# Performance work log

Measured on AMD Instinct MI355X. Metric: run time of the kernel, lower is better.

Reference implementation:

```python
import jax, jax.numpy as jnp
import numpy as np

# Tap offsets (dy, dx) within the 3x3 footprint for each kernel_type.
# kernel_type 0 -> 5-tap skeleton (center + 4-neighbors), 1 -> full 3x3, else -> 3-tap row.
TAPS = {
    0: [(1, 1), (0, 1), (1, 0), (1, 2), (2, 1)],
    1: [(i, j) for i in range(3) for j in range(3)],
    2: [(1, 0), (1, 1), (1, 2)],
}

KERNEL_TYPE = 0
STRIDE = 1
PAD = 1
DIL = 1
SPATIAL = False


def setup_inputs() -> dict:
    key = jax.random.key(0)
    k1, k2 = jax.random.split(key)
    N, Ci, H, W = 16, 256, 64, 64
    Co, K = 256, len(TAPS[KERNEL_TYPE])
    x = jax.random.normal(k1, (N, Ci, H, W), dtype=jnp.float32)
    # kaiming-uniform-ish scale
    bound = np.sqrt(6.0 / (Ci * K))
    weight = jax.random.uniform(k2, (Co, Ci, K), dtype=jnp.float32, minval=-bound, maxval=bound)
    return {"x": x, "weight": weight, "step": 0}


def _spatial_conv(x, weight):
    # x: [N, Ci, H, W], weight: [Co, Ci, K]
    taps = TAPS[KERNEL_TYPE]
    N, Ci, H, W = x.shape
    Hout = (H + 2 * PAD - (DIL * 2 + 1)) // STRIDE + 1
    Wout = (W + 2 * PAD - (DIL * 2 + 1)) // STRIDE + 1
    xp = jnp.pad(x, ((0, 0), (0, 0), (PAD, PAD), (PAD, PAD)))
    outs = []
    for k, (dy, dx) in enumerate(taps):
        y0, x0 = dy * DIL, dx * DIL
        xs = xp[:, :, y0:y0 + (Hout - 1) * STRIDE + 1:STRIDE,
                      x0:x0 + (Wout - 1) * STRIDE + 1:STRIDE]  # [N, Ci, Hout, Wout]
        outs.append(jnp.einsum('nchw,oc->nohw', xs, weight[:, :, k]))
    return jnp.stack(outs, axis=0)  # [K, N, Co, Hout, Wout]


def reference(x, weight, step):
    out = _spatial_conv(x, weight)  # [K, N, Co, H, W]
    if SPATIAL:
        K, N, Co, Ho, Wo = out.shape
        out = jnp.transpose(out, (1, 0, 2, 3, 4)).reshape(N, K * Co, Ho, Wo)
    else:
        out = out.sum(axis=0)  # sum over taps -> [N, Co, H, W]
    return out
```

## Files before the change

kernel.cpp:

```cpp
#include <hip/hip_runtime.h>
#include <hip/hip_bf16.h>
#include <cstddef>

#define N_  16
#define CI  256
#define CO  256
#define KT  5

#define XBUF_B   16896
#define WOFF     33792
#define WBUF_B   40960
#define SMEM_B   115712

typedef __attribute__((ext_vector_type(8)))  short  short8;
typedef __attribute__((ext_vector_type(8)))  unsigned short ushort8;
typedef __attribute__((ext_vector_type(4)))  unsigned int uint4v;
typedef __attribute__((ext_vector_type(16))) float  floatx16;

static __device__ __forceinline__ unsigned short f2bf(float f) {
    union { float f; unsigned u; } v; v.f = f;
    unsigned r = v.u + 0x7fff + ((v.u >> 16) & 1);
    return (unsigned short)(r >> 16);
}

typedef const __attribute__((address_space(1))) unsigned int g_u32;
typedef __attribute__((address_space(3))) unsigned int l_u32;
static __device__ __forceinline__ void gload_lds16(const void* g, void* l) {
    __builtin_amdgcn_global_load_lds((g_u32*)g, (l_u32*)l, 16, 0, 0);
}

__global__ void wtrans_kernel(const float* __restrict__ w, unsigned short* __restrict__ wb) {
    int idx = blockIdx.x * 256 + threadIdx.x;
    if (idx >= KT * CO * CI) return;
    int e  = idx & 7;
    int o  = (idx >> 3) & 255;
    int lh = (idx >> 11) & 1;
    int ks = (idx >> 12) & 1;
    int c  = (idx >> 13) & 7;
    int k  = idx >> 16;
    int ci = c * 32 + ks * 16 + lh * 8 + e;
    wb[idx] = f2bf(w[(size_t)o * (CI * KT) + ci * KT + k]);
}

template<int KS>
static __device__ __forceinline__ void compute_half(const char* wB, const char* xB,
                                                    floatx16 (&acc)[2][2]) {
    #pragma unroll
    for (int k = 0; k < KT; ++k) {
        const int dy = (k == 1) ? 0 : (k == 4) ? 2 : 1;
        const int dx = (k == 2) ? 0 : (k == 3) ? 2 : 1;
        const short8 a0 = *(const short8*)(wB + k * 8192);
        const short8 a1 = *(const short8*)(wB + k * 8192 + 512);
        const short8 b0 = *(const short8*)(xB + (dy * 264 + KS * 132 + dx) * 16);
        const short8 b1 = *(const short8*)(xB + (dy * 264 + KS * 132 + 32 + dx) * 16);
        acc[0][0] = __builtin_amdgcn_mfma_f32_32x32x16_bf16(a0, b0, acc[0][0], 0, 0, 0);
        acc[1][0] = __builtin_amdgcn_mfma_f32_32x32x16_bf16(a1, b0, acc[1][0], 0, 0, 0);
        acc[0][1] = __builtin_amdgcn_mfma_f32_32x32x16_bf16(a0, b1, acc[0][1], 0, 0, 0);
        acc[1][1] = __builtin_amdgcn_mfma_f32_32x32x16_bf16(a1, b1, acc[1][1], 0, 0, 0);
    }
}

__global__ __launch_bounds__(512, 2) void conv_mfma(const float* __restrict__ x,
                                                    const unsigned short* __restrict__ wb,
                                                    float* __restrict__ out) {
    extern __shared__ char smem[];

    const int tid = threadIdx.x;
    const int bx0 = blockIdx.x;
    const int bx  = (bx0 & 7) * 64 + (bx0 >> 3);
    const int g   = bx & 31;
    const int n   = bx >> 5;
    const int h0  = g * 2;

    const int lane  = tid & 63;
    const int wv    = tid >> 6;
    const int l31   = lane & 31;
    const int lh    = lane >> 5;
    const int owave = (wv & 3) * 64;
    const int hrow  = wv >> 2;

    const int sw  = tid & 63;
    const int scg = (tid >> 6) & 3;
    const int sr2 = tid >> 8;

    if (tid < 64) {
        int buf = tid & 1;
        int wp  = ((tid >> 1) & 1) * 65;
        int cg  = (tid >> 2) & 3;
        int r   = (tid >> 4) & 3;
        ((ushort8*)smem)[buf * 1056 + r * 264 + cg * 66 + wp] = (ushort8)0;
    }

    const float* xn = x + (size_t)n * CI * 4096;

    float zm[2];
    int   hcl[2];
    #pragma unroll
    for (int ii = 0; ii < 2; ++ii) {
        int hh = h0 - 1 + sr2 * 2 + ii;
        zm[ii]  = ((unsigned)hh < 64u) ? 1.f : 0.f;
        hcl[ii] = hh < 0 ? 0 : (hh > 63 ? 63 : hh);
    }

    float xr[2][8];
    auto load_chunk = [&](int c) {
        #pragma unroll
        for (int ii = 0; ii < 2; ++ii) {
            const float* p = xn + (c * 32 + scg * 8) * 4096 + hcl[ii] * 64 + sw;
            #pragma unroll
            for (int e = 0; e < 8; ++e) xr[ii][e] = p[e * 4096];
        }
    };
    auto write_chunk = [&](int b) {
        #pragma unroll
        for (int ii = 0; ii < 2; ++ii) {
            const int i = sr2 * 2 + ii;
            uint4v v;
            #pragma unroll
            for (int e = 0; e < 4; ++e) {
                __hip_bfloat162 pk = __float22bfloat162_rn(
                    make_float2(zm[ii] * xr[ii][2 * e], zm[ii] * xr[ii][2 * e + 1]));
                union { __hip_bfloat162 h; unsigned u; } cv; cv.h = pk;
                v[e] = cv.u;
            }
            *(uint4v*)&((ushort8*)smem)[b * 1056 + i * 264 + scg * 66 + (sw + 1)] = v;
        }
    };
    auto stage_w = [&](int c, int ks, int buf) {
        const char* src = (const char*)wb + c * 16384 + ks * 8192 + wv * 1024 + lane * 16;
        char* dst = smem + WOFF + buf * WBUF_B + wv * 1024;
        #pragma unroll
        for (int i = 0; i < 5; ++i)
            gload_lds16(src + (size_t)i * 131072, dst + i * 8192);
    };

    floatx16 acc[2][2];
    #pragma unroll
    for (int ot = 0; ot < 2; ++ot)
        #pragma unroll
        for (int t = 0; t < 2; ++t)
            #pragma unroll
            for (int e = 0; e < 16; ++e) acc[ot][t][e] = 0.f;

    const char* xbase = smem + hrow * 4224 + lh * 1056 + l31 * 16;
    const char* wbase = smem + WOFF + lh * 4096 + (owave + l31) * 16;

    stage_w(0, 0, 0);
    load_chunk(0);
    write_chunk(0);
    __builtin_amdgcn_sched_barrier(0);
    asm volatile("s_waitcnt vmcnt(0) lgkmcnt(0)" ::: "memory");
    __builtin_amdgcn_s_barrier();
    __builtin_amdgcn_sched_barrier(0);

    for (int c = 0; c < 8; ++c) {
        const char* xb = xbase + (c & 1) * XBUF_B;

        stage_w(c, 1, 1);
        asm volatile("" ::: "memory");
        if (c < 7) load_chunk(c + 1);
        asm volatile("" ::: "memory");
        compute_half<0>(wbase, xb, acc);
        __builtin_amdgcn_sched_barrier(0);
        if (c < 7) asm volatile("s_waitcnt vmcnt(16) lgkmcnt(0)" ::: "memory");
        else       asm volatile("s_waitcnt vmcnt(0) lgkmcnt(0)"  ::: "memory");
        __builtin_amdgcn_s_barrier();
        __builtin_amdgcn_sched_barrier(0);

        if (c < 7) stage_w(c + 1, 0, 0);
        asm volatile("" ::: "memory");
        if (c < 7) write_chunk((c + 1) & 1);
        asm volatile("" ::: "memory");
        compute_half<1>(wbase + WBUF_B, xb, acc);
        __builtin_amdgcn_sched_barrier(0);
        if (c < 7) {
            asm volatile("s_waitcnt vmcnt(0) lgkmcnt(0)" ::: "memory");
            __builtin_amdgcn_s_barrier();
            __builtin_amdgcn_sched_barrier(0);
        }
    }

    const int h = h0 + hrow;
    #pragma unroll
    for (int ot = 0; ot < 2; ++ot) {
        #pragma unroll
        for (int wh = 0; wh < 2; ++wh) {
            #pragma unroll
            for (int reg = 0; reg < 16; ++reg) {
                int o = owave + ot * 32 + (reg & 3) + 8 * (reg >> 2) + 4 * lh;
                out[(((size_t)n * CO + o) * 64 + h) * 64 + wh * 32 + l31] = acc[ot][wh][reg];
            }
        }
    }
}

extern "C" void kernel_launch(void* const* d_in, const int* in_sizes, int n_in,
                              void* d_out, int out_size, void* d_ws, size_t ws_size,
                              hipStream_t stream) {
    const float* x = (const float*)d_in[0];
    const float* w = (const float*)d_in[1];
    float* out = (float*)d_out;

    unsigned short* wb = (unsigned short*)d_ws;

    static bool attr_set = false;
    if (!attr_set) {
        hipFuncSetAttribute(reinterpret_cast<const void*>(conv_mfma),
                            hipFuncAttributeMaxDynamicSharedMemorySize, SMEM_B);
        attr_set = true;
    }

    wtrans_kernel<<<dim3((KT * CO * CI + 255) / 256), dim3(256), 0, stream>>>(w, wb);
    conv_mfma<<<dim3(N_ * 32), dim3(512), SMEM_B, stream>>>(x, wb, out);
}
```

Baseline: 148.7 us.

## Split output channels across two blocks of 256 threads with contiguous weight staging

Each block now covers 128 output channels instead of 256, so there are twice as many blocks, each with 4 waves and a smaller LDS footprint (weight buffer halved). The weight pre-transform uses a new layout that keeps each block's per-chunk weights contiguous, so staging issues consecutive 1 KB loads. Compute phases also raise wave priority with s_setprio. The trade-off is that each block reads the input rows twice as often, and per-thread input staging doubles, which raises VGPR use and global traffic for x.

```diff
diff --git a/kernel.cpp b/kernel.cpp
--- a/kernel.cpp
+++ b/kernel.cpp
@@ -9,8 +9,8 @@
 
 #define XBUF_B   16896
 #define WOFF     33792
-#define WBUF_B   40960
-#define SMEM_B   115712
+#define WBUF_B   20480
+#define SMEM_B   74752
 
 typedef __attribute__((ext_vector_type(8)))  short  short8;
 typedef __attribute__((ext_vector_type(8)))  unsigned short ushort8;
@@ -32,14 +32,18 @@
 __global__ void wtrans_kernel(const float* __restrict__ w, unsigned short* __restrict__ wb) {
     int idx = blockIdx.x * 256 + threadIdx.x;
     if (idx >= KT * CO * CI) return;
-    int e  = idx & 7;
-    int o  = (idx >> 3) & 255;
-    int lh = (idx >> 11) & 1;
-    int ks = (idx >> 12) & 1;
-    int c  = (idx >> 13) & 7;
-    int k  = idx >> 16;
-    int ci = c * 32 + ks * 16 + lh * 8 + e;
-    wb[idx] = f2bf(w[(size_t)o * (CI * KT) + ci * KT + k]);
+    int e    = idx & 7;
+    int o7   = (idx >> 3) & 127;
+    int lh   = (idx >> 10) & 1;
+    int rest = idx >> 11;
+    int tap  = rest % 5;
+    int r2   = rest / 5;
+    int ks   = r2 & 1;
+    int c    = (r2 >> 1) & 7;
+    int oh   = r2 >> 4;
+    int ci   = c * 32 + ks * 16 + lh * 8 + e;
+    int o    = oh * 128 + o7;
+    wb[idx] = f2bf(w[(size_t)o * (CI * KT) + ci * KT + tap]);
 }
 
 template<int KS>
@@ -49,8 +53,8 @@
     for (int k = 0; k < KT; ++k) {
         const int dy = (k == 1) ? 0 : (k == 4) ? 2 : 1;
         const int dx = (k == 2) ? 0 : (k == 3) ? 2 : 1;
-        const short8 a0 = *(const short8*)(wB + k * 8192);
-        const short8 a1 = *(const short8*)(wB + k * 8192 + 512);
+        const short8 a0 = *(const short8*)(wB + k * 4096);
+        const short8 a1 = *(const short8*)(wB + k * 4096 + 512);
         const short8 b0 = *(const short8*)(xB + (dy * 264 + KS * 132 + dx) * 16);
         const short8 b1 = *(const short8*)(xB + (dy * 264 + KS * 132 + 32 + dx) * 16);
         acc[0][0] = __builtin_amdgcn_mfma_f32_32x32x16_bf16(a0, b0, acc[0][0], 0, 0, 0);
@@ -60,28 +64,28 @@
     }
 }
 
-__global__ __launch_bounds__(512, 2) void conv_mfma(const float* __restrict__ x,
+__global__ __launch_bounds__(256, 2) void conv_mfma(const float* __restrict__ x,
                                                     const unsigned short* __restrict__ wb,
                                                     float* __restrict__ out) {
     extern __shared__ char smem[];
 
     const int tid = threadIdx.x;
     const int bx0 = blockIdx.x;
-    const int bx  = (bx0 & 7) * 64 + (bx0 >> 3);
-    const int g   = bx & 31;
-    const int n   = bx >> 5;
+    const int bx  = (bx0 & 7) * 128 + (bx0 >> 3);
+    const int oh  = bx & 1;
+    const int g   = (bx >> 1) & 31;
+    const int n   = bx >> 6;
     const int h0  = g * 2;
 
     const int lane  = tid & 63;
     const int wv    = tid >> 6;
     const int l31   = lane & 31;
     const int lh    = lane >> 5;
-    const int owave = (wv & 3) * 64;
-    const int hrow  = wv >> 2;
+    const int owave = (wv & 1) * 64;
+    const int hrow  = wv >> 1;
 
     const int sw  = tid & 63;
     const int scg = (tid >> 6) & 3;
-    const int sr2 = tid >> 8;
 
     if (tid < 64) {
         int buf = tid & 1;
@@ -93,19 +97,19 @@
 
     const float* xn = x + (size_t)n * CI * 4096;
 
-    float zm[2];
-    int   hcl[2];
-    #pragma unroll
-    for (int ii = 0; ii < 2; ++ii) {
-        int hh = h0 - 1 + sr2 * 2 + ii;
+    float zm[4];
+    int   hcl[4];
+    #pragma unroll
+    for (int ii = 0; ii < 4; ++ii) {
+        int hh = h0 - 1 + ii;
         zm[ii]  = ((unsigned)hh < 64u) ? 1.f : 0.f;
         hcl[ii] = hh < 0 ? 0 : (hh > 63 ? 63 : hh);
     }
 
-    float xr[2][8];
+    float xr[4][8];
     auto load_chunk = [&](int c) {
         #pragma unroll
-        for (int ii = 0; ii < 2; ++ii) {
+        for (int ii = 0; ii < 4; ++ii) {
             const float* p = xn + (c * 32 + scg * 8) * 4096 + hcl[ii] * 64 + sw;
             #pragma unroll
             for (int e = 0; e < 8; ++e) xr[ii][e] = p[e * 4096];
@@ -113,8 +117,7 @@
     };
     auto write_chunk = [&](int b) {
         #pragma unroll
-        for (int ii = 0; ii < 2; ++ii) {
-            const int i = sr2 * 2 + ii;
+        for (int ii = 0; ii < 4; ++ii) {
             uint4v v;
             #pragma unroll
             for (int e = 0; e < 4; ++e) {
@@ -123,15 +126,16 @@
                 union { __hip_bfloat162 h; unsigned u; } cv; cv.h = pk;
                 v[e] = cv.u;
             }
-            *(uint4v*)&((ushort8*)smem)[b * 1056 + i * 264 + scg * 66 + (sw + 1)] = v;
+            *(uint4v*)&((ushort8*)smem)[b * 1056 + ii * 264 + scg * 66 + (sw + 1)] = v;
         }
     };
     auto stage_w = [&](int c, int ks, int buf) {
-        const char* src = (const char*)wb + c * 16384 + ks * 8192 + wv * 1024 + lane * 16;
-        char* dst = smem + WOFF + buf * WBUF_B + wv * 1024;
+        const char* src = (const char*)wb + oh * 327680 + c * 40960 + ks * 20480
+                          + wv * 5120 + lane * 16;
+        char* dst = smem + WOFF + buf * WBUF_B + wv * 5120;
         #pragma unroll
         for (int i = 0; i < 5; ++i)
-            gload_lds16(src + (size_t)i * 131072, dst + i * 8192);
+            gload_lds16(src + i * 1024, dst + i * 1024);
     };
 
     floatx16 acc[2][2];
@@ -143,7 +147,7 @@
             for (int e = 0; e < 16; ++e) acc[ot][t][e] = 0.f;
 
     const char* xbase = smem + hrow * 4224 + lh * 1056 + l31 * 16;
-    const char* wbase = smem + WOFF + lh * 4096 + (owave + l31) * 16;
+    const char* wbase = smem + WOFF + lh * 2048 + (owave + l31) * 16;
 
     stage_w(0, 0, 0);
     load_chunk(0);
@@ -160,9 +164,11 @@
         asm volatile("" ::: "memory");
         if (c < 7) load_chunk(c + 1);
         asm volatile("" ::: "memory");
+        __builtin_amdgcn_s_setprio(1);
         compute_half<0>(wbase, xb, acc);
+        __builtin_amdgcn_s_setprio(0);
         __builtin_amdgcn_sched_barrier(0);
-        if (c < 7) asm volatile("s_waitcnt vmcnt(16) lgkmcnt(0)" ::: "memory");
+        if (c < 7) asm volatile("s_waitcnt vmcnt(32) lgkmcnt(0)" ::: "memory");
         else       asm volatile("s_waitcnt vmcnt(0) lgkmcnt(0)"  ::: "memory");
         __builtin_amdgcn_s_barrier();
         __builtin_amdgcn_sched_barrier(0);
@@ -171,7 +177,9 @@
         asm volatile("" ::: "memory");
         if (c < 7) write_chunk((c + 1) & 1);
         asm volatile("" ::: "memory");
+        __builtin_amdgcn_s_setprio(1);
         compute_half<1>(wbase + WBUF_B, xb, acc);
+        __builtin_amdgcn_s_setprio(0);
         __builtin_amdgcn_sched_barrier(0);
         if (c < 7) {
             asm volatile("s_waitcnt vmcnt(0) lgkmcnt(0)" ::: "memory");
@@ -187,7 +195,7 @@
         for (int wh = 0; wh < 2; ++wh) {
             #pragma unroll
             for (int reg = 0; reg < 16; ++reg) {
-                int o = owave + ot * 32 + (reg & 3) + 8 * (reg >> 2) + 4 * lh;
+                int o = oh * 128 + owave + ot * 32 + (reg & 3) + 8 * (reg >> 2) + 4 * lh;
                 out[(((size_t)n * CO + o) * 64 + h) * 64 + wh * 32 + l31] = acc[ot][wh][reg];
             }
         }
@@ -211,5 +219,5 @@
     }
 
     wtrans_kernel<<<dim3((KT * CO * CI + 255) / 256), dim3(256), 0, stream>>>(w, wb);
-    conv_mfma<<<dim3(N_ * 32), dim3(512), SMEM_B, stream>>>(x, wb, out);
-}
+    conv_mfma<<<dim3(N_ * 32 * 2), dim3(256), SMEM_B, stream>>>(x, wb, out);
+}
```

New measurement: 154.4 us. +3.8%, slower.

## Compute four output rows per block to reuse staged weights across rows

Applied to the files above, without the earlier changes.

Each block now covers four output rows instead of two, and each wave holds accumulators for two rows. Every weight fragment read from LDS therefore feeds twice as many MFMAs, and the per-block weight staging from global memory is amortized over twice the output. The trade-offs are a 256-block grid (fewer blocks than before, which may underfill the CUs), larger LDS use at 132 KB that likely limits residency to one block per CU, and double the accumulator registers.

```diff
diff --git a/kernel.cpp b/kernel.cpp
--- a/kernel.cpp
+++ b/kernel.cpp
@@ -7,10 +7,10 @@
 #define CO  256
 #define KT  5
 
-#define XBUF_B   16896
-#define WOFF     33792
+#define XBUF_B   25344
+#define WOFF     50688
 #define WBUF_B   40960
-#define SMEM_B   115712
+#define SMEM_B   132608
 
 typedef __attribute__((ext_vector_type(8)))  short  short8;
 typedef __attribute__((ext_vector_type(8)))  unsigned short ushort8;
@@ -44,19 +44,23 @@
 
 template<int KS>
 static __device__ __forceinline__ void compute_half(const char* wB, const char* xB,
-                                                    floatx16 (&acc)[2][2]) {
+                                                    floatx16 (&acc)[2][2][2]) {
     #pragma unroll
     for (int k = 0; k < KT; ++k) {
         const int dy = (k == 1) ? 0 : (k == 4) ? 2 : 1;
         const int dx = (k == 2) ? 0 : (k == 3) ? 2 : 1;
         const short8 a0 = *(const short8*)(wB + k * 8192);
         const short8 a1 = *(const short8*)(wB + k * 8192 + 512);
-        const short8 b0 = *(const short8*)(xB + (dy * 264 + KS * 132 + dx) * 16);
-        const short8 b1 = *(const short8*)(xB + (dy * 264 + KS * 132 + 32 + dx) * 16);
-        acc[0][0] = __builtin_amdgcn_mfma_f32_32x32x16_bf16(a0, b0, acc[0][0], 0, 0, 0);
-        acc[1][0] = __builtin_amdgcn_mfma_f32_32x32x16_bf16(a1, b0, acc[1][0], 0, 0, 0);
-        acc[0][1] = __builtin_amdgcn_mfma_f32_32x32x16_bf16(a0, b1, acc[0][1], 0, 0, 0);
-        acc[1][1] = __builtin_amdgcn_mfma_f32_32x32x16_bf16(a1, b1, acc[1][1], 0, 0, 0);
+        #pragma unroll
+        for (int hr = 0; hr < 2; ++hr) {
+            #pragma unroll
+            for (int wh = 0; wh < 2; ++wh) {
+                const short8 b = *(const short8*)(xB +
+                    ((hr + dy) * 264 + KS * 132 + wh * 32 + dx) * 16);
+                acc[0][hr][wh] = __builtin_amdgcn_mfma_f32_32x32x16_bf16(a0, b, acc[0][hr][wh], 0, 0, 0);
+                acc[1][hr][wh] = __builtin_amdgcn_mfma_f32_32x32x16_bf16(a1, b, acc[1][hr][wh], 0, 0, 0);
+            }
+        }
     }
 }
 
@@ -67,45 +71,45 @@
 
     const int tid = threadIdx.x;
     const int bx0 = blockIdx.x;
-    const int bx  = (bx0 & 7) * 64 + (bx0 >> 3);
-    const int g   = bx & 31;
-    const int n   = bx >> 5;
-    const int h0  = g * 2;
-
-    const int lane  = tid & 63;
-    const int wv    = tid >> 6;
-    const int l31   = lane & 31;
-    const int lh    = lane >> 5;
-    const int owave = (wv & 3) * 64;
-    const int hrow  = wv >> 2;
+    const int bx  = (bx0 & 7) * 32 + (bx0 >> 3);
+    const int hq  = bx & 15;
+    const int n   = bx >> 4;
+    const int h0  = hq * 4;
+
+    const int lane    = tid & 63;
+    const int wv      = tid >> 6;
+    const int l31     = lane & 31;
+    const int lh      = lane >> 5;
+    const int owave   = (wv & 3) * 64;
+    const int rowbase = (wv >> 2) * 2;
 
     const int sw  = tid & 63;
     const int scg = (tid >> 6) & 3;
-    const int sr2 = tid >> 8;
-
-    if (tid < 64) {
+    const int sr3 = tid >> 8;
+
+    if (tid < 96) {
         int buf = tid & 1;
         int wp  = ((tid >> 1) & 1) * 65;
         int cg  = (tid >> 2) & 3;
-        int r   = (tid >> 4) & 3;
-        ((ushort8*)smem)[buf * 1056 + r * 264 + cg * 66 + wp] = (ushort8)0;
+        int r   = tid >> 4;
+        ((ushort8*)smem)[buf * 1584 + r * 264 + cg * 66 + wp] = (ushort8)0;
     }
 
     const float* xn = x + (size_t)n * CI * 4096;
 
-    float zm[2];
-    int   hcl[2];
-    #pragma unroll
-    for (int ii = 0; ii < 2; ++ii) {
-        int hh = h0 - 1 + sr2 * 2 + ii;
+    float zm[3];
+    int   hcl[3];
+    #pragma unroll
+    for (int ii = 0; ii < 3; ++ii) {
+        int hh = h0 - 1 + sr3 * 3 + ii;
         zm[ii]  = ((unsigned)hh < 64u) ? 1.f : 0.f;
         hcl[ii] = hh < 0 ? 0 : (hh > 63 ? 63 : hh);
     }
 
-    float xr[2][8];
+    float xr[3][8];
     auto load_chunk = [&](int c) {
         #pragma unroll
-        for (int ii = 0; ii < 2; ++ii) {
+        for (int ii = 0; ii < 3; ++ii) {
             const float* p = xn + (c * 32 + scg * 8) * 4096 + hcl[ii] * 64 + sw;
             #pragma unroll
             for (int e = 0; e < 8; ++e) xr[ii][e] = p[e * 4096];
@@ -113,8 +117,8 @@
     };
     auto write_chunk = [&](int b) {
         #pragma unroll
-        for (int ii = 0; ii < 2; ++ii) {
-            const int i = sr2 * 2 + ii;
+        for (int ii = 0; ii < 3; ++ii) {
+            const int i = sr3 * 3 + ii;
             uint4v v;
             #pragma unroll
             for (int e = 0; e < 4; ++e) {
@@ -123,7 +127,7 @@
                 union { __hip_bfloat162 h; unsigned u; } cv; cv.h = pk;
                 v[e] = cv.u;
             }
-            *(uint4v*)&((ushort8*)smem)[b * 1056 + i * 264 + scg * 66 + (sw + 1)] = v;
+            *(uint4v*)&((ushort8*)smem)[b * 1584 + i * 264 + scg * 66 + (sw + 1)] = v;
         }
     };
     auto stage_w = [&](int c, int ks, int buf) {
@@ -134,15 +138,17 @@
             gload_lds16(src + (size_t)i * 131072, dst + i * 8192);
     };
 
-    floatx16 acc[2][2];
+    floatx16 acc[2][2][2];
     #pragma unroll
     for (int ot = 0; ot < 2; ++ot)
         #pragma unroll
-        for (int t = 0; t < 2; ++t)
-            #pragma unroll
-            for (int e = 0; e < 16; ++e) acc[ot][t][e] = 0.f;
-
-    const char* xbase = smem + hrow * 4224 + lh * 1056 + l31 * 16;
+        for (int hr = 0; hr < 2; ++hr)
+            #pragma unroll
+            for (int wh = 0; wh < 2; ++wh)
+                #pragma unroll
+                for (int e = 0; e < 16; ++e) acc[ot][hr][wh][e] = 0.f;
+
+    const char* xbase = smem + rowbase * 4224 + lh * 1056 + l31 * 16;
     const char* wbase = smem + WOFF + lh * 4096 + (owave + l31) * 16;
 
     stage_w(0, 0, 0);
@@ -162,7 +168,7 @@
         asm volatile("" ::: "memory");
         compute_half<0>(wbase, xb, acc);
         __builtin_amdgcn_sched_barrier(0);
-        if (c < 7) asm volatile("s_waitcnt vmcnt(16) lgkmcnt(0)" ::: "memory");
+        if (c < 7) asm volatile("s_waitcnt vmcnt(24) lgkmcnt(0)" ::: "memory");
         else       asm volatile("s_waitcnt vmcnt(0) lgkmcnt(0)"  ::: "memory");
         __builtin_amdgcn_s_barrier();
         __builtin_amdgcn_sched_barrier(0);
@@ -180,15 +186,18 @@
         }
     }
 
-    const int h = h0 + hrow;
     #pragma unroll
     for (int ot = 0; ot < 2; ++ot) {
         #pragma unroll
-        for (int wh = 0; wh < 2; ++wh) {
-            #pragma unroll
-            for (int reg = 0; reg < 16; ++reg) {
-                int o = owave + ot * 32 + (reg & 3) + 8 * (reg >> 2) + 4 * lh;
-                out[(((size_t)n * CO + o) * 64 + h) * 64 + wh * 32 + l31] = acc[ot][wh][reg];
+        for (int hr = 0; hr < 2; ++hr) {
+            const int h = h0 + rowbase + hr;
+            #pragma unroll
+            for (int wh = 0; wh < 2; ++wh) {
+                #pragma unroll
+                for (int reg = 0; reg < 16; ++reg) {
+                    int o = owave + ot * 32 + (reg & 3) + 8 * (reg >> 2) + 4 * lh;
+                    out[(((size_t)n * CO + o) * 64 + h) * 64 + wh * 32 + l31] = acc[ot][hr][wh][reg];
+                }
             }
         }
     }
@@ -211,5 +220,5 @@
     }
 
     wtrans_kernel<<<dim3((KT * CO * CI + 255) / 256), dim3(256), 0, stream>>>(w, wb);
-    conv_mfma<<<dim3(N_ * 32), dim3(512), SMEM_B, stream>>>(x, wb, out);
-}
+    conv_mfma<<<dim3(N_ * 16), dim3(512), SMEM_B, stream>>>(x, wb, out);
+}
```

Result: faster. 137.0 us (-7.9%).
